# Kernel tuning notes

Measured on AMD Instinct MI355X. Metric: run time of the kernel, lower is better.

## Reference

```python
import jax, jax.numpy as jnp
import numpy as np

N_NODES = 100000
N_EDGES = 1000000
HID = 128


def setup_inputs() -> dict:
    key = jax.random.key(0)
    ks = jax.random.split(key, 8)
    z = jax.random.normal(ks[0], (N_NODES, HID), dtype=jnp.float32)
    edge_index = jax.random.randint(ks[1], (2, N_EDGES), 0, N_NODES, dtype=jnp.int64)
    # Linear params: W stored as [out, in] like torch; init ~ kaiming-uniform-ish scale
    W1 = jax.random.normal(ks[2], (256, 2 * HID), dtype=jnp.float32) * (1.0 / np.sqrt(2 * HID))
    b1 = jnp.zeros((256,), dtype=jnp.float32)
    W2 = jax.random.normal(ks[3], (64, 256), dtype=jnp.float32) * (1.0 / np.sqrt(256))
    b2 = jnp.zeros((64,), dtype=jnp.float32)
    W3 = jax.random.normal(ks[4], (1, 64), dtype=jnp.float32) * (1.0 / np.sqrt(64))
    b3 = jnp.zeros((1,), dtype=jnp.float32)
    return {"z": z, "edge_index": edge_index, "W1": W1, "b1": b1,
            "W2": W2, "b2": b2, "W3": W3, "b3": b3}


def reference(z, edge_index, W1, b1, W2, b2, W3, b3):
    # gather src/dst node embeddings and concat -> [E, 2*HID]
    src = z[edge_index[0]]
    dst = z[edge_index[1]]
    edge_feats = jnp.concatenate([src, dst], axis=1)
    # 3-layer MLP with leaky_relu(0.2); dropout is identity in eval mode
    h = jax.nn.leaky_relu(edge_feats @ W1.T + b1, negative_slope=0.2)
    h = jax.nn.leaky_relu(h @ W2.T + b2, negative_slope=0.2)
    return h @ W3.T + b3  # [E, 1]
```

## Files before the change

### kernel.cpp

```cpp
#include <hip/hip_runtime.h>
#include <hip/hip_bf16.h>

typedef __attribute__((ext_vector_type(8))) short bf16x8;
typedef __attribute__((ext_vector_type(4))) float f32x4;

#define HID    128
#define KDIM   256
#define MT     64

__device__ __forceinline__ unsigned short f2bf(float x) {
    unsigned int u = __float_as_uint(x);
    u += 0x7FFFu + ((u >> 16) & 1u);
    return (unsigned short)(u >> 16);
}
__device__ __forceinline__ int pack2(float a, float b) {
    return (int)f2bf(a) | ((int)f2bf(b) << 16);
}
__device__ __forceinline__ float lrelu(float x) { return fmaxf(x, 0.2f * x); }

__global__ void convert_all_kernel(const float* __restrict__ z,
                                   const float* __restrict__ W1,
                                   const float* __restrict__ W2,
                                   unsigned short* __restrict__ zb,
                                   unsigned short* __restrict__ w1b,
                                   unsigned short* __restrict__ w2b,
                                   int nz4, int nw14, int nw24) {
    int total = nz4 + nw14 + nw24;
    for (int i = blockIdx.x * blockDim.x + threadIdx.x; i < total;
         i += gridDim.x * blockDim.x) {
        const float4* src;
        unsigned short* dst;
        int j;
        if (i < nz4)             { src = (const float4*)z;  dst = zb;  j = i; }
        else if (i < nz4 + nw14) { src = (const float4*)W1; dst = w1b; j = i - nz4; }
        else                     { src = (const float4*)W2; dst = w2b; j = i - nz4 - nw14; }
        float4 v = src[j];
        ushort4 o;
        o.x = f2bf(v.x); o.y = f2bf(v.y); o.z = f2bf(v.z); o.w = f2bf(v.w);
        *(ushort4*)(dst + (size_t)j * 4) = o;
    }
}

__global__ void convert_w_kernel(const float* __restrict__ W1,
                                 const float* __restrict__ W2,
                                 unsigned short* __restrict__ w1b,
                                 unsigned short* __restrict__ w2b,
                                 int nw14, int nw24) {
    int i = blockIdx.x * blockDim.x + threadIdx.x;
    if (i >= nw14 + nw24) return;
    const float4* src;
    unsigned short* dst;
    int j;
    if (i < nw14) { src = (const float4*)W1; dst = w1b; j = i; }
    else          { src = (const float4*)W2; dst = w2b; j = i - nw14; }
    float4 v = src[j];
    ushort4 o;
    o.x = f2bf(v.x); o.y = f2bf(v.y); o.z = f2bf(v.z); o.w = f2bf(v.w);
    *(ushort4*)(dst + (size_t)j * 4) = o;
}

template <bool ZB>
__global__ __launch_bounds__(256, 4)
void disc_kernel(const float* __restrict__ z,
                 const unsigned short* __restrict__ zb,
                 const int* __restrict__ ei,
                 const unsigned short* __restrict__ w1b,
                 const float* __restrict__ b1,
                 const unsigned short* __restrict__ w2b,
                 const float* __restrict__ b2,
                 const float* __restrict__ W3,
                 const float* __restrict__ b3,
                 float* __restrict__ out, int E) {
    __shared__ __align__(16) unsigned char smem[32768];

    const int tid  = threadIdx.x;
    const int wave = tid >> 6;
    const int lane = tid & 63;
    const int lr   = lane & 15;
    const int lk   = lane >> 4;
    const int e0   = blockIdx.x * MT;
    const float b3s = b3[0];

    if constexpr (ZB) {
        #pragma unroll
        for (int t = 0; t < 8; ++t) {
            int row = wave * 16 + t * 2 + (lane >> 5);
            int e = e0 + row; if (e >= E) e = E - 1;
            int s = ei[e];
            int d = ei[E + e];
            int c = (lane & 31) ^ (row & 7);
            int node = (c < 16) ? s : d;
            const unsigned short* g = zb + (size_t)node * HID + (c & 15) * 8;
            __builtin_amdgcn_global_load_lds(
                (const __attribute__((address_space(1))) unsigned int*)g,
                (__attribute__((address_space(3))) unsigned int*)(smem + wave * 8192 + t * 1024),
                16, 0, 0);
        }
    } else {
        int r = tid >> 2, q = tid & 3;
        int e = e0 + r; if (e >= E) e = E - 1;
        int s = ei[e];
        int d = ei[E + e];
        const float4* zs = (const float4*)(z + (size_t)s * HID);
        const float4* zd = (const float4*)(z + (size_t)d * HID);
        const int swz = (r & 7) << 4;
        #pragma unroll
        for (int j = 0; j < 8; ++j) {
            int c = q * 8 + j;
            const float4* src = (c < 16) ? (zs + c * 2) : (zd + (c - 16) * 2);
            float4 v0 = src[0], v1 = src[1];
            int4 o;
            o.x = pack2(v0.x, v0.y);
            o.y = pack2(v0.z, v0.w);
            o.z = pack2(v1.x, v1.y);
            o.w = pack2(v1.z, v1.w);
            *(int4*)(smem + r * 512 + ((c * 16) ^ swz)) = o;
        }
    }

    const int n0 = wave * 64;
    const unsigned short* wbase = w1b + (size_t)(n0 + lr) * KDIM + lk * 8;
    bf16x8 bcur[4], bnxt[4];
    #pragma unroll
    for (int ni = 0; ni < 4; ++ni)
        bcur[ni] = *(const bf16x8*)(wbase + (size_t)ni * 16 * KDIM);

    __syncthreads();

    f32x4 acc[4][4];
    #pragma unroll
    for (int mi = 0; mi < 4; ++mi)
        #pragma unroll
        for (int ni = 0; ni < 4; ++ni)
            acc[mi][ni] = (f32x4){0.f, 0.f, 0.f, 0.f};

    #pragma unroll
    for (int ks = 0; ks < 8; ++ks) {
        if (ks < 7) {
            #pragma unroll
            for (int ni = 0; ni < 4; ++ni)
                bnxt[ni] = *(const bf16x8*)(wbase + (size_t)ni * 16 * KDIM + (ks + 1) * 32);
        }
        const int kb = ks * 64 + lk * 16;
        bf16x8 a[4];
        #pragma unroll
        for (int mi = 0; mi < 4; ++mi) {
            int row = mi * 16 + lr;
            a[mi] = *(const bf16x8*)(smem + row * 512 + (kb ^ ((row & 7) << 4)));
        }
        #pragma unroll
        for (int mi = 0; mi < 4; ++mi)
            #pragma unroll
            for (int ni = 0; ni < 4; ++ni)
                acc[mi][ni] = __builtin_amdgcn_mfma_f32_16x16x32_bf16(
                    bcur[ni], a[mi], acc[mi][ni], 0, 0, 0);
        if (ks < 7) {
            #pragma unroll
            for (int ni = 0; ni < 4; ++ni) bcur[ni] = bnxt[ni];
        }
    }

    const int c2 = wave * 16 + lr;
    const unsigned short* w2base = w2b + (size_t)c2 * KDIM + lk * 8;
    bf16x8 bwc = *(const bf16x8*)(w2base);

    __syncthreads();

    #pragma unroll
    for (int ni = 0; ni < 4; ++ni) {
        int colb = n0 + ni * 16 + lk * 4;
        float4 bias = *(const float4*)(b1 + colb);
        #pragma unroll
        for (int mi = 0; mi < 4; ++mi) {
            int row = mi * 16 + lr;
            float x0 = lrelu(acc[mi][ni][0] + bias.x);
            float x1 = lrelu(acc[mi][ni][1] + bias.y);
            float x2 = lrelu(acc[mi][ni][2] + bias.z);
            float x3 = lrelu(acc[mi][ni][3] + bias.w);
            int2 o;
            o.x = pack2(x0, x1);
            o.y = pack2(x2, x3);
            *(int2*)(smem + row * 512 + ((colb * 2) ^ ((row & 7) << 4))) = o;
        }
    }
    __syncthreads();

    f32x4 acc2[4];
    #pragma unroll
    for (int mi = 0; mi < 4; ++mi) acc2[mi] = (f32x4){0.f, 0.f, 0.f, 0.f};
    bf16x8 bwn;
    #pragma unroll
    for (int ks = 0; ks < 8; ++ks) {
        if (ks < 7) bwn = *(const bf16x8*)(w2base + (ks + 1) * 32);
        const int kb = ks * 64 + lk * 16;
        bf16x8 a2[4];
        #pragma unroll
        for (int mi = 0; mi < 4; ++mi) {
            int row = mi * 16 + lr;
            a2[mi] = *(const bf16x8*)(smem + row * 512 + (kb ^ ((row & 7) << 4)));
        }
        #pragma unroll
        for (int mi = 0; mi < 4; ++mi)
            acc2[mi] = __builtin_amdgcn_mfma_f32_16x16x32_bf16(
                bwc, a2[mi], acc2[mi], 0, 0, 0);
        if (ks < 7) bwc = bwn;
    }
    __syncthreads();

    float* part = (float*)smem;
    {
        int colb = wave * 16 + lk * 4;
        float4 b2v = *(const float4*)(b2 + colb);
        float4 w3v = *(const float4*)(W3 + colb);
        #pragma unroll
        for (int mi = 0; mi < 4; ++mi) {
            float s = lrelu(acc2[mi][0] + b2v.x) * w3v.x
                    + lrelu(acc2[mi][1] + b2v.y) * w3v.y
                    + lrelu(acc2[mi][2] + b2v.z) * w3v.z
                    + lrelu(acc2[mi][3] + b2v.w) * w3v.w;
            s += __shfl_xor(s, 16);
            s += __shfl_xor(s, 32);
            if (lk == 0) part[wave * 64 + mi * 16 + lr] = s;
        }
    }
    __syncthreads();

    if (tid < MT) {
        int e = e0 + tid;
        float s = part[tid] + part[64 + tid] + part[128 + tid] + part[192 + tid] + b3s;
        if (e < E) out[e] = s;
    }
}

extern "C" void kernel_launch(void* const* d_in, const int* in_sizes, int n_in,
                              void* d_out, int out_size, void* d_ws, size_t ws_size,
                              hipStream_t stream) {
    const float* z  = (const float*)d_in[0];
    const int*   ei = (const int*)d_in[1];
    const float* W1 = (const float*)d_in[2];
    const float* b1 = (const float*)d_in[3];
    const float* W2 = (const float*)d_in[4];
    const float* b2 = (const float*)d_in[5];
    const float* W3 = (const float*)d_in[6];
    const float* b3 = (const float*)d_in[7];
    float* out = (float*)d_out;

    const int nz  = in_sizes[0];
    const int E   = in_sizes[1] / 2;
    const int nw1 = in_sizes[2];
    const int nw2 = in_sizes[4];

    const size_t need_full = (size_t)(nz + nw1 + nw2) * 2;
    const bool zb_ok = ws_size >= need_full;

    const int blocks = (E + MT - 1) / MT;

    if (zb_ok) {
        unsigned short* zbp = (unsigned short*)d_ws;
        unsigned short* w1b = zbp + nz;
        unsigned short* w2b = w1b + nw1;
        convert_all_kernel<<<2048, 256, 0, stream>>>(z, W1, W2, zbp, w1b, w2b,
                                                     nz / 4, nw1 / 4, nw2 / 4);
        disc_kernel<true><<<blocks, 256, 0, stream>>>(z, zbp, ei, w1b, b1, w2b,
                                                      b2, W3, b3, out, E);
    } else {
        unsigned short* w1b = (unsigned short*)d_ws;
        unsigned short* w2b = w1b + nw1;
        const int ntot = (nw1 + nw2) / 4;
        convert_w_kernel<<<(ntot + 255) / 256, 256, 0, stream>>>(W1, W2, w1b, w2b,
                                                                 nw1 / 4, nw2 / 4);
        disc_kernel<false><<<blocks, 256, 0, stream>>>(z, (const unsigned short*)nullptr,
                                                       ei, w1b, b1, w2b, b2, W3, b3,
                                                       out, E);
    }
}
```

Measured before the change: 408.5 us.

## Make disc kernel persistent with double-buffered LDS gather prefetch

Converts the per-tile kernel into a persistent grid-stride loop over a fixed grid of 512 blocks. The LDS is double-buffered (64KB) so the next tile's edge indices and gathered embeddings are issued while the current tile runs its MFMA layers. Raw s_barrier with manual waitcnt replaces __syncthreads. In exchange it cuts occupancy to two blocks per CU and relies on careful hand placement of barriers and waits to keep it correct.

```diff
diff --git a/kernel.cpp b/kernel.cpp
--- a/kernel.cpp
+++ b/kernel.cpp
@@ -60,7 +60,7 @@
 }
 
 template <bool ZB>
-__global__ __launch_bounds__(256, 4)
+__global__ __launch_bounds__(256, 2)
 void disc_kernel(const float* __restrict__ z,
                  const unsigned short* __restrict__ zb,
                  const int* __restrict__ ei,
@@ -71,164 +71,217 @@
                  const float* __restrict__ W3,
                  const float* __restrict__ b3,
                  float* __restrict__ out, int E) {
-    __shared__ __align__(16) unsigned char smem[32768];
+    __shared__ __align__(16) unsigned char smem[65536];
 
     const int tid  = threadIdx.x;
     const int wave = tid >> 6;
     const int lane = tid & 63;
     const int lr   = lane & 15;
     const int lk   = lane >> 4;
-    const int e0   = blockIdx.x * MT;
     const float b3s = b3[0];
-
-    if constexpr (ZB) {
-        #pragma unroll
-        for (int t = 0; t < 8; ++t) {
-            int row = wave * 16 + t * 2 + (lane >> 5);
-            int e = e0 + row; if (e >= E) e = E - 1;
-            int s = ei[e];
-            int d = ei[E + e];
-            int c = (lane & 31) ^ (row & 7);
-            int node = (c < 16) ? s : d;
-            const unsigned short* g = zb + (size_t)node * HID + (c & 15) * 8;
-            __builtin_amdgcn_global_load_lds(
-                (const __attribute__((address_space(1))) unsigned int*)g,
-                (__attribute__((address_space(3))) unsigned int*)(smem + wave * 8192 + t * 1024),
-                16, 0, 0);
-        }
-    } else {
-        int r = tid >> 2, q = tid & 3;
-        int e = e0 + r; if (e >= E) e = E - 1;
-        int s = ei[e];
-        int d = ei[E + e];
-        const float4* zs = (const float4*)(z + (size_t)s * HID);
-        const float4* zd = (const float4*)(z + (size_t)d * HID);
-        const int swz = (r & 7) << 4;
-        #pragma unroll
-        for (int j = 0; j < 8; ++j) {
-            int c = q * 8 + j;
-            const float4* src = (c < 16) ? (zs + c * 2) : (zd + (c - 16) * 2);
-            float4 v0 = src[0], v1 = src[1];
-            int4 o;
-            o.x = pack2(v0.x, v0.y);
-            o.y = pack2(v0.z, v0.w);
-            o.z = pack2(v1.x, v1.y);
-            o.w = pack2(v1.z, v1.w);
-            *(int4*)(smem + r * 512 + ((c * 16) ^ swz)) = o;
-        }
-    }
+    const int ntiles = (E + MT - 1) / MT;
+    const int stride = gridDim.x;
 
     const int n0 = wave * 64;
-    const unsigned short* wbase = w1b + (size_t)(n0 + lr) * KDIM + lk * 8;
-    bf16x8 bcur[4], bnxt[4];
-    #pragma unroll
-    for (int ni = 0; ni < 4; ++ni)
-        bcur[ni] = *(const bf16x8*)(wbase + (size_t)ni * 16 * KDIM);
-
-    __syncthreads();
-
-    f32x4 acc[4][4];
-    #pragma unroll
-    for (int mi = 0; mi < 4; ++mi)
-        #pragma unroll
-        for (int ni = 0; ni < 4; ++ni)
-            acc[mi][ni] = (f32x4){0.f, 0.f, 0.f, 0.f};
-
-    #pragma unroll
-    for (int ks = 0; ks < 8; ++ks) {
-        if (ks < 7) {
-            #pragma unroll
-            for (int ni = 0; ni < 4; ++ni)
-                bnxt[ni] = *(const bf16x8*)(wbase + (size_t)ni * 16 * KDIM + (ks + 1) * 32);
-        }
-        const int kb = ks * 64 + lk * 16;
-        bf16x8 a[4];
-        #pragma unroll
-        for (int mi = 0; mi < 4; ++mi) {
-            int row = mi * 16 + lr;
-            a[mi] = *(const bf16x8*)(smem + row * 512 + (kb ^ ((row & 7) << 4)));
-        }
-        #pragma unroll
-        for (int mi = 0; mi < 4; ++mi)
-            #pragma unroll
-            for (int ni = 0; ni < 4; ++ni)
-                acc[mi][ni] = __builtin_amdgcn_mfma_f32_16x16x32_bf16(
-                    bcur[ni], a[mi], acc[mi][ni], 0, 0, 0);
-        if (ks < 7) {
-            #pragma unroll
-            for (int ni = 0; ni < 4; ++ni) bcur[ni] = bnxt[ni];
-        }
-    }
-
+    const unsigned short* wbase  = w1b + (size_t)(n0 + lr) * KDIM + lk * 8;
     const int c2 = wave * 16 + lr;
     const unsigned short* w2base = w2b + (size_t)c2 * KDIM + lk * 8;
-    bf16x8 bwc = *(const bf16x8*)(w2base);
-
-    __syncthreads();
-
-    #pragma unroll
-    for (int ni = 0; ni < 4; ++ni) {
-        int colb = n0 + ni * 16 + lk * 4;
-        float4 bias = *(const float4*)(b1 + colb);
-        #pragma unroll
-        for (int mi = 0; mi < 4; ++mi) {
-            int row = mi * 16 + lr;
-            float x0 = lrelu(acc[mi][ni][0] + bias.x);
-            float x1 = lrelu(acc[mi][ni][1] + bias.y);
-            float x2 = lrelu(acc[mi][ni][2] + bias.z);
-            float x3 = lrelu(acc[mi][ni][3] + bias.w);
-            int2 o;
-            o.x = pack2(x0, x1);
-            o.y = pack2(x2, x3);
-            *(int2*)(smem + row * 512 + ((colb * 2) ^ ((row & 7) << 4))) = o;
-        }
-    }
-    __syncthreads();
-
-    f32x4 acc2[4];
-    #pragma unroll
-    for (int mi = 0; mi < 4; ++mi) acc2[mi] = (f32x4){0.f, 0.f, 0.f, 0.f};
-    bf16x8 bwn;
-    #pragma unroll
-    for (int ks = 0; ks < 8; ++ks) {
-        if (ks < 7) bwn = *(const bf16x8*)(w2base + (ks + 1) * 32);
-        const int kb = ks * 64 + lk * 16;
-        bf16x8 a2[4];
-        #pragma unroll
-        for (int mi = 0; mi < 4; ++mi) {
-            int row = mi * 16 + lr;
-            a2[mi] = *(const bf16x8*)(smem + row * 512 + (kb ^ ((row & 7) << 4)));
-        }
+
+    int sArr[8], dArr[8];
+
+    auto load_ei = [&](int t) {
+        if constexpr (ZB) {
+            #pragma unroll
+            for (int tt = 0; tt < 8; ++tt) {
+                int row = wave * 16 + tt * 2 + (lane >> 5);
+                int e = t * MT + row; if (e >= E) e = E - 1;
+                sArr[tt] = ei[e];
+                dArr[tt] = ei[E + e];
+            }
+        } else {
+            int r = tid >> 2;
+            int e = t * MT + r; if (e >= E) e = E - 1;
+            sArr[0] = ei[e];
+            dArr[0] = ei[E + e];
+        }
+    };
+
+    auto stage = [&](unsigned char* base) {
+        if constexpr (ZB) {
+            #pragma unroll
+            for (int tt = 0; tt < 8; ++tt) {
+                int row = wave * 16 + tt * 2 + (lane >> 5);
+                int c = (lane & 31) ^ (row & 7);
+                int node = (c < 16) ? sArr[tt] : dArr[tt];
+                const unsigned short* g = zb + (size_t)node * HID + (c & 15) * 8;
+                __builtin_amdgcn_global_load_lds(
+                    (const __attribute__((address_space(1))) unsigned int*)g,
+                    (__attribute__((address_space(3))) unsigned int*)(base + wave * 8192 + tt * 1024),
+                    16, 0, 0);
+            }
+        } else {
+            int r = tid >> 2, q = tid & 3;
+            const float4* zs = (const float4*)(z + (size_t)sArr[0] * HID);
+            const float4* zd = (const float4*)(z + (size_t)dArr[0] * HID);
+            const int swz = (r & 7) << 4;
+            #pragma unroll
+            for (int j = 0; j < 8; ++j) {
+                int c = q * 8 + j;
+                const float4* src = (c < 16) ? (zs + c * 2) : (zd + (c - 16) * 2);
+                float4 v0 = src[0], v1 = src[1];
+                int4 o;
+                o.x = pack2(v0.x, v0.y);
+                o.y = pack2(v0.z, v0.w);
+                o.z = pack2(v1.x, v1.y);
+                o.w = pack2(v1.z, v1.w);
+                *(int4*)(base + r * 512 + ((c * 16) ^ swz)) = o;
+            }
+        }
+    };
+
+    int tile = blockIdx.x;
+    if (tile >= ntiles) return;
+
+    load_ei(tile);
+    stage(smem);
+    int cur = 0;
+
+    for (;;) {
+        unsigned char* X = smem + (cur << 15);
+        unsigned char* Y = smem + ((cur ^ 1) << 15);
+        const int e0 = tile * MT;
+
+        asm volatile("s_waitcnt vmcnt(0) lgkmcnt(0)" ::: "memory");
+        __builtin_amdgcn_s_barrier();
+        __builtin_amdgcn_sched_barrier(0);
+
+        const int ntile = tile + stride;
+        const bool has = ntile < ntiles;
+        if (has) load_ei(ntile);
+
+        f32x4 acc[4][4];
         #pragma unroll
         for (int mi = 0; mi < 4; ++mi)
-            acc2[mi] = __builtin_amdgcn_mfma_f32_16x16x32_bf16(
-                bwc, a2[mi], acc2[mi], 0, 0, 0);
-        if (ks < 7) bwc = bwn;
-    }
-    __syncthreads();
-
-    float* part = (float*)smem;
-    {
-        int colb = wave * 16 + lk * 4;
-        float4 b2v = *(const float4*)(b2 + colb);
-        float4 w3v = *(const float4*)(W3 + colb);
-        #pragma unroll
-        for (int mi = 0; mi < 4; ++mi) {
-            float s = lrelu(acc2[mi][0] + b2v.x) * w3v.x
-                    + lrelu(acc2[mi][1] + b2v.y) * w3v.y
-                    + lrelu(acc2[mi][2] + b2v.z) * w3v.z
-                    + lrelu(acc2[mi][3] + b2v.w) * w3v.w;
-            s += __shfl_xor(s, 16);
-            s += __shfl_xor(s, 32);
-            if (lk == 0) part[wave * 64 + mi * 16 + lr] = s;
-        }
-    }
-    __syncthreads();
-
-    if (tid < MT) {
-        int e = e0 + tid;
-        float s = part[tid] + part[64 + tid] + part[128 + tid] + part[192 + tid] + b3s;
-        if (e < E) out[e] = s;
+            #pragma unroll
+            for (int ni = 0; ni < 4; ++ni)
+                acc[mi][ni] = (f32x4){0.f, 0.f, 0.f, 0.f};
+
+        bf16x8 bcur[4], bnxt[4];
+        #pragma unroll
+        for (int ni = 0; ni < 4; ++ni)
+            bcur[ni] = *(const bf16x8*)(wbase + (size_t)ni * 16 * KDIM);
+
+        #pragma unroll
+        for (int ks = 0; ks < 8; ++ks) {
+            if (ks < 7) {
+                #pragma unroll
+                for (int ni = 0; ni < 4; ++ni)
+                    bnxt[ni] = *(const bf16x8*)(wbase + (size_t)ni * 16 * KDIM + (ks + 1) * 32);
+            }
+            const int kb = ks * 64 + lk * 16;
+            bf16x8 a[4];
+            #pragma unroll
+            for (int mi = 0; mi < 4; ++mi) {
+                int row = mi * 16 + lr;
+                a[mi] = *(const bf16x8*)(X + row * 512 + (kb ^ ((row & 7) << 4)));
+            }
+            #pragma unroll
+            for (int mi = 0; mi < 4; ++mi)
+                #pragma unroll
+                for (int ni = 0; ni < 4; ++ni)
+                    acc[mi][ni] = __builtin_amdgcn_mfma_f32_16x16x32_bf16(
+                        bcur[ni], a[mi], acc[mi][ni], 0, 0, 0);
+            if (ks < 7) {
+                #pragma unroll
+                for (int ni = 0; ni < 4; ++ni) bcur[ni] = bnxt[ni];
+            }
+        }
+
+        bf16x8 w2r[8];
+        #pragma unroll
+        for (int ks = 0; ks < 8; ++ks)
+            w2r[ks] = *(const bf16x8*)(w2base + ks * 32);
+
+        if (has) stage(Y);
+
+        asm volatile("" ::: "memory");
+        __builtin_amdgcn_s_barrier();
+        __builtin_amdgcn_sched_barrier(0);
+
+        #pragma unroll
+        for (int ni = 0; ni < 4; ++ni) {
+            int colb = n0 + ni * 16 + lk * 4;
+            float4 bias = *(const float4*)(b1 + colb);
+            #pragma unroll
+            for (int mi = 0; mi < 4; ++mi) {
+                int row = mi * 16 + lr;
+                float x0 = lrelu(acc[mi][ni][0] + bias.x);
+                float x1 = lrelu(acc[mi][ni][1] + bias.y);
+                float x2 = lrelu(acc[mi][ni][2] + bias.z);
+                float x3 = lrelu(acc[mi][ni][3] + bias.w);
+                int2 o;
+                o.x = pack2(x0, x1);
+                o.y = pack2(x2, x3);
+                *(int2*)(X + row * 512 + ((colb * 2) ^ ((row & 7) << 4))) = o;
+            }
+        }
+
+        asm volatile("s_waitcnt lgkmcnt(0)" ::: "memory");
+        __builtin_amdgcn_s_barrier();
+        __builtin_amdgcn_sched_barrier(0);
+
+        f32x4 acc2[4];
+        #pragma unroll
+        for (int mi = 0; mi < 4; ++mi) acc2[mi] = (f32x4){0.f, 0.f, 0.f, 0.f};
+        #pragma unroll
+        for (int ks = 0; ks < 8; ++ks) {
+            const int kb = ks * 64 + lk * 16;
+            bf16x8 a2[4];
+            #pragma unroll
+            for (int mi = 0; mi < 4; ++mi) {
+                int row = mi * 16 + lr;
+                a2[mi] = *(const bf16x8*)(X + row * 512 + (kb ^ ((row & 7) << 4)));
+            }
+            #pragma unroll
+            for (int mi = 0; mi < 4; ++mi)
+                acc2[mi] = __builtin_amdgcn_mfma_f32_16x16x32_bf16(
+                    w2r[ks], a2[mi], acc2[mi], 0, 0, 0);
+        }
+
+        asm volatile("" ::: "memory");
+        __builtin_amdgcn_s_barrier();
+        __builtin_amdgcn_sched_barrier(0);
+
+        float* part = (float*)X;
+        {
+            int colb = wave * 16 + lk * 4;
+            float4 b2v = *(const float4*)(b2 + colb);
+            float4 w3v = *(const float4*)(W3 + colb);
+            #pragma unroll
+            for (int mi = 0; mi < 4; ++mi) {
+                float s = lrelu(acc2[mi][0] + b2v.x) * w3v.x
+                        + lrelu(acc2[mi][1] + b2v.y) * w3v.y
+                        + lrelu(acc2[mi][2] + b2v.z) * w3v.z
+                        + lrelu(acc2[mi][3] + b2v.w) * w3v.w;
+                s += __shfl_xor(s, 16);
+                s += __shfl_xor(s, 32);
+                if (lk == 0) part[wave * 64 + mi * 16 + lr] = s;
+            }
+        }
+
+        asm volatile("s_waitcnt lgkmcnt(0)" ::: "memory");
+        __builtin_amdgcn_s_barrier();
+        __builtin_amdgcn_sched_barrier(0);
+
+        if (tid < MT) {
+            int e = e0 + tid;
+            float s = part[tid] + part[64 + tid] + part[128 + tid] + part[192 + tid] + b3s;
+            if (e < E) out[e] = s;
+        }
+
+        if (!has) break;
+        tile = ntile;
+        cur ^= 1;
     }
 }
 
@@ -253,7 +306,7 @@
     const size_t need_full = (size_t)(nz + nw1 + nw2) * 2;
     const bool zb_ok = ws_size >= need_full;
 
-    const int blocks = (E + MT - 1) / MT;
+    const int grid = 512;
 
     if (zb_ok) {
         unsigned short* zbp = (unsigned short*)d_ws;
@@ -261,16 +314,16 @@
         unsigned short* w2b = w1b + nw1;
         convert_all_kernel<<<2048, 256, 0, stream>>>(z, W1, W2, zbp, w1b, w2b,
                                                      nz / 4, nw1 / 4, nw2 / 4);
-        disc_kernel<true><<<blocks, 256, 0, stream>>>(z, zbp, ei, w1b, b1, w2b,
-                                                      b2, W3, b3, out, E);
+        disc_kernel<true><<<grid, 256, 0, stream>>>(z, zbp, ei, w1b, b1, w2b,
+                                                    b2, W3, b3, out, E);
     } else {
         unsigned short* w1b = (unsigned short*)d_ws;
         unsigned short* w2b = w1b + nw1;
         const int ntot = (nw1 + nw2) / 4;
         convert_w_kernel<<<(ntot + 255) / 256, 256, 0, stream>>>(W1, W2, w1b, w2b,
                                                                  nw1 / 4, nw2 / 4);
-        disc_kernel<false><<<blocks, 256, 0, stream>>>(z, (const unsigned short*)nullptr,
-                                                       ei, w1b, b1, w2b, b2, W3, b3,
-                                                       out, E);
+        disc_kernel<false><<<grid, 256, 0, stream>>>(z, (const unsigned short*)nullptr,
+                                                     ei, w1b, b1, w2b, b2, W3, b3,
+                                                     out, E);
     }
 }
```

Result: slower. 441.0 us (+7.9%).
